# Performance work log

Measured on AMD Instinct MI355X. Metric: run time of the kernel, lower is better.

The kernel has to match this reference:

```python
import jax, jax.numpy as jnp
import numpy as np

N_NODES = 50000
N_RELS = 50
N_CLASSES = 40
EMB_DIM = 16
RP = 16
N_TRIPLES = 400000


def setup_inputs() -> dict:
    rng = np.random.default_rng(0)
    s = rng.integers(0, N_NODES, size=N_TRIPLES)
    r = rng.integers(0, N_RELS, size=N_TRIPLES)
    o = rng.integers(0, N_NODES, size=N_TRIPLES)
    # unique (s,o) pairs, as in torch.unique(pairs, dim=0, return_inverse=True)
    pairs = np.stack([s, o], axis=1)
    unique_pairs, inverse = np.unique(pairs, axis=0, return_inverse=True)
    nt = unique_pairs.shape[0]
    # relation_matrix COO (nt, num_rels), coalesced (duplicate (row,col) summed)
    keys = inverse.astype(np.int64) * N_RELS + r
    uk, counts = np.unique(keys, return_counts=True)
    rm_rows = (uk // N_RELS).astype(np.int32)
    rm_cols = (uk % N_RELS).astype(np.int32)
    rm_vals = counts.astype(np.float32)
    # hindices / vindices exactly as in __init__ (note o*rm / s*rm construction)
    s_u = unique_pairs[:, 0].astype(np.int64)
    o_u = unique_pairs[:, 1].astype(np.int64)
    rm = np.arange(RP, dtype=np.int64)[:, None]            # (rp, 1)
    h_rows = np.broadcast_to(s_u[None, :], (RP, nt)).reshape(-1).astype(np.int32)
    h_cols = (o_u[None, :] * rm).reshape(-1).astype(np.int32)
    v_rows = (s_u[None, :] * rm).reshape(-1).astype(np.int32)
    v_cols = np.broadcast_to(o_u[None, :], (RP, nt)).reshape(-1).astype(np.int32)
    # float params (xavier-like scale for weights, randn for rel emb, zero biases)
    key = jax.random.key(0)
    k1, k2, k3 = jax.random.split(key, 3)
    gain = np.sqrt(2.0)  # relu gain
    w1_std = gain * np.sqrt(2.0 / (N_NODES + EMB_DIM))
    w2_std = gain * np.sqrt(2.0 / (EMB_DIM + N_CLASSES))
    return {
        'rel_emb': jax.random.normal(k1, (N_RELS, RP), dtype=jnp.float32),
        'weights1': jax.random.normal(k2, (RP, N_NODES, EMB_DIM), dtype=jnp.float32) * w1_std,
        'weights2': jax.random.normal(k3, (RP, EMB_DIM, N_CLASSES), dtype=jnp.float32) * w2_std,
        'bias1': jnp.zeros((EMB_DIM,), dtype=jnp.float32),
        'bias2': jnp.zeros((N_CLASSES,), dtype=jnp.float32),
        'rm_rows': jnp.asarray(rm_rows),
        'rm_cols': jnp.asarray(rm_cols),
        'rm_vals': jnp.asarray(rm_vals),
        'h_rows': jnp.asarray(h_rows),
        'h_cols': jnp.asarray(h_cols),
        'v_rows': jnp.asarray(v_rows),
        'v_cols': jnp.asarray(v_cols),
    }


def reference(rel_emb, weights1, weights2, bias1, bias2,
              rm_rows, rm_cols, rm_vals, h_rows, h_cols, v_rows, v_cols):
    rp, n, e = weights1.shape
    nt = h_rows.shape[0] // rp
    # latents = sparse.mm(relation_matrix, relation_embeddings) -> (nt, rp)
    latents = jax.ops.segment_sum(rm_vals[:, None] * rel_emb[rm_cols], rm_rows,
                                  num_segments=nt)
    latents = jax.nn.softmax(latents, axis=1)
    lf = latents.T.reshape(-1)                              # (rp*nt,)
    # sum_sparse(hindices, lf, (n, n*rp), row=False): per-column sums, gathered
    colsum = jax.ops.segment_sum(lf, h_cols, num_segments=n * rp)
    ln = lf / colsum[h_cols]
    # spmm(hindices, ln, (n, n*rp), weights1_flat) -> (n, e)
    w1f = weights1.reshape(rp * n, e)
    h = jax.ops.segment_sum(ln[:, None] * w1f[h_cols], h_rows, num_segments=n)
    h = jax.nn.relu(h + bias1)
    # sum_sparse(vindices, lf, (n*rp, n), row=True): per-row sums, gathered
    rowsum = jax.ops.segment_sum(lf, v_rows, num_segments=n * rp)
    ln2 = lf / rowsum[v_rows]
    # spmm(vindices, ln2, (n*rp, n), h) -> (n*rp, e)
    h2 = jax.ops.segment_sum(ln2[:, None] * h[v_cols], v_rows, num_segments=n * rp)
    h2 = h2.reshape(rp, n, e)
    out = jnp.einsum('rhc,rnh->nc', weights2, h2) + bias2
    return out
```

## Files before the change

### kernel.cpp

```cpp
#include <hip/hip_runtime.h>

#define RP 16
#define EMB 16
#define NC 40

#define BCASTF(dst, srci, R) \
    dst = __int_as_float(__builtin_amdgcn_mov_dpp(srci, 0x150 + R, 0xf, 0xf, true));

__global__ void k_count(const int* __restrict__ s_u, const int* __restrict__ o_u,
                        int* __restrict__ cnt_s, int* __restrict__ cnt_o, int nt) {
    int t = blockIdx.x * blockDim.x + threadIdx.x;
    if (t < nt) {
        atomicAdd(&cnt_s[s_u[t]], 1);
        atomicAdd(&cnt_o[o_u[t]], 1);
    }
}

__global__ void k_scan_blk(const int* __restrict__ cnt_s, int* __restrict__ offs_s,
                           const int* __restrict__ cnt_o, int* __restrict__ offs_o,
                           int* __restrict__ partials, int n, int nblk) {
    const int* in = blockIdx.y ? cnt_o : cnt_s;
    int* out = blockIdx.y ? offs_o : offs_s;
    int tid = threadIdx.x;
    int i0 = blockIdx.x * 1024 + tid * 4;
    int v[4];
    #pragma unroll
    for (int q = 0; q < 4; ++q) {
        int i = i0 + q;
        v[q] = (i < n) ? in[i] : 0;
    }
    int tsum = v[0] + v[1] + v[2] + v[3];
    int lane = tid & 63, wid = tid >> 6;
    int x = tsum;
    #pragma unroll
    for (int d = 1; d < 64; d <<= 1) {
        int u = __shfl_up(x, d, 64);
        if (lane >= d) x += u;
    }
    __shared__ int wsum[4];
    if (lane == 63) wsum[wid] = x;
    __syncthreads();
    int woff = 0;
    for (int wq = 0; wq < wid; ++wq) woff += wsum[wq];
    int run = woff + x - tsum;
    #pragma unroll
    for (int q = 0; q < 4; ++q) {
        int i = i0 + q;
        if (i < n) out[i] = run;
        run += v[q];
    }
    if (tid == 255) partials[blockIdx.y * nblk + blockIdx.x] = run;
}

__global__ void k_scan_top(int* __restrict__ partials, int nblk) {
    int w = threadIdx.x >> 6;
    int lane = threadIdx.x & 63;
    int carry = 0;
    for (int base = 0; base < nblk; base += 64) {
        int idx = base + lane;
        int v = (idx < nblk) ? partials[w * nblk + idx] : 0;
        int x = v;
        #pragma unroll
        for (int d = 1; d < 64; d <<= 1) {
            int u = __shfl_up(x, d, 64);
            if (lane >= d) x += u;
        }
        if (idx < nblk) partials[w * nblk + idx] = carry + x - v;
        carry += __shfl(x, 63, 64);
    }
}

__global__ void k_scan_add(int* __restrict__ offs_s, int* __restrict__ cur_s,
                           int* __restrict__ offs_o, int* __restrict__ cur_o,
                           const int* __restrict__ partials, int n, int nblk) {
    int* out = blockIdx.y ? offs_o : offs_s;
    int* cur = blockIdx.y ? cur_o : cur_s;
    int add = partials[blockIdx.y * nblk + blockIdx.x];
    int i0 = blockIdx.x * 1024 + threadIdx.x * 4;
    #pragma unroll
    for (int q = 0; q < 4; ++q) {
        int i = i0 + q;
        if (i < n) {
            int vv = out[i] + add;
            out[i] = vv;
            cur[i] = vv;
        }
    }
}

__global__ void k_latents(const float* __restrict__ rel_emb,
                          const int* __restrict__ rows,
                          const int* __restrict__ cols,
                          const float* __restrict__ vals,
                          const int* __restrict__ s_u,
                          const int* __restrict__ o_u,
                          int* __restrict__ cur_o,
                          float* __restrict__ lat_t, float* __restrict__ lat_o,
                          float* __restrict__ lat0, int* __restrict__ su_o,
                          int nm) {
    int i = blockIdx.x * blockDim.x + threadIdx.x;
    int e = i >> 4, k = i & 15;
    if (e >= nm) return;
    int row = rows[e];
    if (e > 0 && rows[e - 1] == row) return;
    float acc = vals[e] * rel_emb[cols[e] * RP + k];
    while (e + 1 < nm && rows[e + 1] == row) {
        ++e;
        acc += vals[e] * rel_emb[cols[e] * RP + k];
    }
    float m = acc;
    #pragma unroll
    for (int d = 1; d < 16; d <<= 1) m = fmaxf(m, __shfl_xor(m, d, 16));
    float v = expf(acc - m);
    float s = v;
    #pragma unroll
    for (int d = 1; d < 16; d <<= 1) s += __shfl_xor(s, d, 16);
    v = v / s;
    lat_t[(size_t)row * RP + k] = v;
    int po = 0;
    if (k == 0) {
        int ou = o_u[row];
        po = atomicAdd(&cur_o[ou], 1);
        su_o[po] = s_u[row];
        lat0[row] = v;
    }
    po = __shfl(po, 0, 16);
    lat_o[(size_t)po * RP + k] = v;
}

__global__ void k_r0(const float* __restrict__ lat0,
                     float* __restrict__ rowsum, float* __restrict__ colsum,
                     int nt) {
    float acc = 0.f;
    for (int t = blockIdx.x * blockDim.x + threadIdx.x; t < nt;
         t += gridDim.x * blockDim.x)
        acc += lat0[t];
    #pragma unroll
    for (int d = 32; d; d >>= 1) acc += __shfl_down(acc, d, 64);
    __shared__ float sm[4];
    int lane = threadIdx.x & 63, wid = threadIdx.x >> 6;
    if (lane == 0) sm[wid] = acc;
    __syncthreads();
    if (threadIdx.x == 0) {
        float tot = sm[0] + sm[1] + sm[2] + sm[3];
        atomicAdd(&rowsum[0], tot);
        atomicAdd(&colsum[0], tot);
    }
}

__global__ void k_latsum(const float* __restrict__ lat_o,
                         const int* __restrict__ offs_o,
                         const int* __restrict__ cnt_o,
                         float* __restrict__ colsum, int n) {
    int i = blockIdx.x * blockDim.x + threadIdx.x;
    int v = i >> 4, k = i & 15;
    if (v >= n) return;
    int beg = offs_o[v], d = cnt_o[v];
    if (d == 0) return;
    float ls = 0.f;
    int j = 0;
    for (; j + 4 <= d; j += 4) {
        float a0 = lat_o[(size_t)(beg + j + 0) * RP + k];
        float a1 = lat_o[(size_t)(beg + j + 1) * RP + k];
        float a2 = lat_o[(size_t)(beg + j + 2) * RP + k];
        float a3 = lat_o[(size_t)(beg + j + 3) * RP + k];
        ls += (a0 + a1) + (a2 + a3);
    }
    for (; j < d; ++j) ls += lat_o[(size_t)(beg + j) * RP + k];
    if (k >= 1) atomicAdd(&colsum[(size_t)v * k], ls);
}

__global__ void k_h_acc(const float* __restrict__ lat_o,
                        const int* __restrict__ offs_o,
                        const int* __restrict__ cnt_o,
                        const int* __restrict__ su_o,
                        const float* __restrict__ colsum,
                        const float* __restrict__ w1,
                        float* __restrict__ h, int n) {
    int i = blockIdx.x * blockDim.x + threadIdx.x;
    int o = i >> 4, k = i & 15;
    if (o >= n) return;
    int d = cnt_o[o];
    if (d == 0) return;
    int beg = offs_o[o];
    float W[RP];
    #pragma unroll
    for (int r = 0; r < RP; ++r)
        W[r] = w1[(size_t)(o * r) * EMB + k];
    float rcp_cs = 1.f / colsum[(size_t)o * k];
    for (int j0 = 0; j0 < d; j0 += 16) {
        int su16 = su_o[beg + min(j0 + k, d - 1)];
        float la[16];
        #pragma unroll
        for (int e = 0; e < 16; ++e)
            la[e] = lat_o[(size_t)(beg + min(j0 + e, d - 1)) * RP + k];
        #pragma unroll
        for (int e = 0; e < 16; ++e) {
            if (j0 + e >= d) break;
            float ln = la[e] * rcp_cs;
            int ln_i = __float_as_int(ln);
            float acc = 0.f, b;
            #define HACC_STEP(R) BCASTF(b, ln_i, R); acc = fmaf(b, W[R], acc);
            HACC_STEP(0)  HACC_STEP(1)  HACC_STEP(2)  HACC_STEP(3)
            HACC_STEP(4)  HACC_STEP(5)  HACC_STEP(6)  HACC_STEP(7)
            HACC_STEP(8)  HACC_STEP(9)  HACC_STEP(10) HACC_STEP(11)
            HACC_STEP(12) HACC_STEP(13) HACC_STEP(14) HACC_STEP(15)
            #undef HACC_STEP
            int s = __shfl(su16, e, 16);
            atomicAdd(&h[s * EMB + k], acc);
        }
    }
}

__global__ void k_h2(const float* __restrict__ lat_t,
                     const int* __restrict__ offs_s,
                     const int* __restrict__ cnt_s,
                     const int* __restrict__ o_u,
                     float* __restrict__ rowsum,
                     const float* __restrict__ h,
                     const float* __restrict__ bias1,
                     float* __restrict__ M2,
                     float* __restrict__ r0part, int n) {
    __shared__ float r0acc[EMB];
    if (threadIdx.x < EMB) r0acc[threadIdx.x] = 0.f;
    __syncthreads();
    int i = blockIdx.x * blockDim.x + threadIdx.x;
    int s = i >> 4, k = i & 15;
    float b1k = bias1[k];
    float M[RP];
    #pragma unroll
    for (int r = 0; r < RP; ++r) M[r] = 0.f;
    float rs_acc = 0.f;
    int d = 0;
    if (s < n) {
        int beg = offs_s[s];
        d = cnt_s[s];
        for (int j0 = 0; j0 < d; j0 += 16) {
            int o16 = o_u[beg + min(j0 + k, d - 1)];
            float hv[16], la[16];
            #pragma unroll
            for (int e = 0; e < 16; ++e) {
                int oe = __shfl(o16, e, 16);
                hv[e] = h[(size_t)oe * EMB + k];
                la[e] = lat_t[(size_t)(beg + min(j0 + e, d - 1)) * RP + k];
            }
            #pragma unroll
            for (int e = 0; e < 16; ++e) {
                if (j0 + e >= d) break;
                float hvr = fmaxf(hv[e] + b1k, 0.f);
                rs_acc += la[e];
                int lat_i = __float_as_int(la[e]);
                float b;
                #define H2_STEP(R) BCASTF(b, lat_i, R); M[R] = fmaf(b, hvr, M[R]);
                H2_STEP(0)  H2_STEP(1)  H2_STEP(2)  H2_STEP(3)
                H2_STEP(4)  H2_STEP(5)  H2_STEP(6)  H2_STEP(7)
                H2_STEP(8)  H2_STEP(9)  H2_STEP(10) H2_STEP(11)
                H2_STEP(12) H2_STEP(13) H2_STEP(14) H2_STEP(15)
                #undef H2_STEP
            }
        }
    }
    if (s < n) {
        if (d > 0) {
            if (k >= 1) atomicAdd(&rowsum[(size_t)s * k], rs_acc);
            atomicAdd(&r0acc[k], M[0]);
        }
        float* dst = &M2[(size_t)s * 15 * EMB + k];
        #pragma unroll
        for (int r = 1; r < RP; ++r)
            dst[(size_t)(r - 1) * EMB] = M[r];
    }
    __syncthreads();
    if (threadIdx.x < EMB)
        r0part[(size_t)blockIdx.x * EMB + threadIdx.x] = r0acc[threadIdx.x];
}

__global__ void k_h2r0(const float* __restrict__ r0part,
                       float* __restrict__ g0, int nblk) {
    __shared__ float red[1024];
    int k = threadIdx.x & 15, j0 = threadIdx.x >> 4;
    float acc = 0.f;
    for (int j = j0; j < nblk; j += 64)
        acc += r0part[(size_t)j * EMB + k];
    red[j0 * 16 + k] = acc;
    __syncthreads();
    #pragma unroll
    for (int st = 32; st >= 1; st >>= 1) {
        if (j0 < st) red[j0 * 16 + k] += red[(j0 + st) * 16 + k];
        __syncthreads();
    }
    if (threadIdx.x < 16) g0[threadIdx.x] = red[threadIdx.x];
}

#define CB2 20
__global__ void k_out(const float* __restrict__ w2,
                      const float* __restrict__ bias2,
                      const float* __restrict__ M2,
                      const float* __restrict__ g0,
                      const float* __restrict__ rowsum,
                      float* __restrict__ out, int n) {
    __shared__ float w2s[RP * EMB * NC];
    for (int i = threadIdx.x; i < RP * EMB * NC; i += 256)
        w2s[i] = w2[i];
    __syncthreads();
    int gi = blockIdx.x * blockDim.x + threadIdx.x;
    int node = gi >> 1;
    int c0 = (gi & 1) * CB2;
    if (node >= n) return;
    float acc[CB2];
    #pragma unroll
    for (int c = 0; c < CB2; ++c) acc[c] = bias2[c0 + c];
    for (int rq = 0; rq < RP; ++rq) {
        int m = rq * n + node;
        float rs = rowsum[m];
        float rcp = (rs != 0.f) ? 1.f / rs : 0.f;
        float hv[EMB];
        #pragma unroll
        for (int q = 0; q < EMB; ++q) hv[q] = 0.f;
        if (m == 0) {
            #pragma unroll
            for (int q = 0; q < EMB; ++q) hv[q] = g0[q];
        }
        #pragma unroll
        for (int r = 1; r < RP; ++r) {
            if (m % r == 0) {
                int s = m / r;
                if (s < n) {
                    const float4* row =
                        (const float4*)&M2[((size_t)s * 15 + (r - 1)) * EMB];
                    #pragma unroll
                    for (int q = 0; q < 4; ++q) {
                        float4 v = row[q];
                        hv[q * 4 + 0] += v.x;
                        hv[q * 4 + 1] += v.y;
                        hv[q * 4 + 2] += v.z;
                        hv[q * 4 + 3] += v.w;
                    }
                }
            }
        }
        #pragma unroll
        for (int hh = 0; hh < EMB; ++hh) {
            const float4* wrow = (const float4*)&w2s[(rq * EMB + hh) * NC + c0];
            float hvv = hv[hh] * rcp;
            #pragma unroll
            for (int q5 = 0; q5 < 5; ++q5) {
                float4 wv = wrow[q5];
                acc[q5 * 4 + 0] += wv.x * hvv;
                acc[q5 * 4 + 1] += wv.y * hvv;
                acc[q5 * 4 + 2] += wv.z * hvv;
                acc[q5 * 4 + 3] += wv.w * hvv;
            }
        }
    }
    float4* op = (float4*)&out[node * NC + c0];
    #pragma unroll
    for (int q5 = 0; q5 < 5; ++q5)
        op[q5] = make_float4(acc[q5 * 4], acc[q5 * 4 + 1],
                             acc[q5 * 4 + 2], acc[q5 * 4 + 3]);
}

extern "C" void kernel_launch(void* const* d_in, const int* in_sizes, int n_in,
                              void* d_out, int out_size, void* d_ws, size_t ws_size,
                              hipStream_t stream) {
    const float* rel_emb = (const float*)d_in[0];
    const float* w1      = (const float*)d_in[1];
    const float* w2      = (const float*)d_in[2];
    const float* b1      = (const float*)d_in[3];
    const float* b2      = (const float*)d_in[4];
    const int*   rm_rows = (const int*)d_in[5];
    const int*   rm_cols = (const int*)d_in[6];
    const float* rm_vals = (const float*)d_in[7];
    const int*   h_rows  = (const int*)d_in[8];
    const int*   v_cols  = (const int*)d_in[11];

    const int nm = in_sizes[5];
    const int ne = in_sizes[8];
    const int nt = ne / RP;
    const int n  = in_sizes[1] / (RP * EMB);

    const int B = 256;
    const int nblk_h2 = (n * 16 + B - 1) / B;
    const int nblk_sc = (n + 1023) / 1024;

    char* w = (char*)d_ws;
    float* colsum = (float*)w;  w += (size_t)n * RP * 4;
    float* rowsum = (float*)w;  w += (size_t)n * RP * 4;
    float* h      = (float*)w;  w += (size_t)n * EMB * 4;
    int* cnt_s    = (int*)w;    w += (size_t)n * 4;
    int* cnt_o    = (int*)w;    w += (size_t)n * 4;
    size_t zero_bytes = (size_t)(w - (char*)d_ws);
    float* M2     = (float*)w;  w += (size_t)n * 15 * EMB * 4;
    float* lat_t  = (float*)w;  w += (size_t)nt * RP * 4;
    float* lat_o  = (float*)w;  w += (size_t)nt * RP * 4;
    float* lat0   = (float*)w;  w += (size_t)nt * 4;
    int* su_o     = (int*)w;    w += (size_t)nt * 4;
    int* offs_s   = (int*)w;    w += (size_t)n * 4;
    int* cur_s    = (int*)w;    w += (size_t)n * 4;
    int* offs_o   = (int*)w;    w += (size_t)n * 4;
    int* cur_o    = (int*)w;    w += (size_t)n * 4;
    float* r0part = (float*)w;  w += (size_t)nblk_h2 * EMB * 4;
    float* g0     = (float*)w;  w += (size_t)EMB * 4;
    int* partials = (int*)w;    w += (size_t)2 * nblk_sc * 4;
    if ((size_t)(w - (char*)d_ws) > ws_size) return;

    hipMemsetAsync(d_ws, 0, zero_bytes, stream);

    k_count<<<dim3((nt + B - 1) / B), dim3(B), 0, stream>>>(
        h_rows, v_cols, cnt_s, cnt_o, nt);
    k_scan_blk<<<dim3(nblk_sc, 2), dim3(B), 0, stream>>>(
        cnt_s, offs_s, cnt_o, offs_o, partials, n, nblk_sc);
    k_scan_top<<<dim3(1), dim3(128), 0, stream>>>(partials, nblk_sc);
    k_scan_add<<<dim3(nblk_sc, 2), dim3(B), 0, stream>>>(
        offs_s, cur_s, offs_o, cur_o, partials, n, nblk_sc);
    k_latents<<<dim3((nm * 16 + B - 1) / B), dim3(B), 0, stream>>>(
        rel_emb, rm_rows, rm_cols, rm_vals, h_rows, v_cols,
        cur_o, lat_t, lat_o, lat0, su_o, nm);
    k_r0<<<dim3(64), dim3(B), 0, stream>>>(lat0, rowsum, colsum, nt);
    k_latsum<<<dim3((n * 16 + B - 1) / B), dim3(B), 0, stream>>>(
        lat_o, offs_o, cnt_o, colsum, n);
    k_h_acc<<<dim3((n * 16 + B - 1) / B), dim3(B), 0, stream>>>(
        lat_o, offs_o, cnt_o, su_o, colsum, w1, h, n);
    k_h2<<<dim3(nblk_h2), dim3(B), 0, stream>>>(
        lat_t, offs_s, cnt_s, v_cols, rowsum, h, b1, M2, r0part, n);
    k_h2r0<<<dim3(1), dim3(1024), 0, stream>>>(r0part, g0, nblk_h2);
    k_out<<<dim3((n * 2 + B - 1) / B), dim3(B), 0, stream>>>(
        w2, b2, M2, g0, rowsum, (float*)d_out, n);
}
```

Measured before the change: 271.9 us.

## Remap k_out to 16 lanes per node with DPP broadcast of hidden values

The output kernel now gives each node 16 threads, one per embedding component, instead of 2 threads that each cover 20 classes. Each lane loads one M2 element, scales it by the reciprocal row sum, and uses DPP row broadcasts to share the 16 hidden values. Each lane then accumulates up to 3 output classes. This cuts per-thread registers and serial FMA work and makes M2 loads coalesced, at the cost of 8x more threads, redundant rowsum and mod/div work per lane, and some idle lanes on the third class.

```diff
diff --git a/kernel.cpp b/kernel.cpp
--- a/kernel.cpp
+++ b/kernel.cpp
@@ -292,7 +292,6 @@
     if (threadIdx.x < 16) g0[threadIdx.x] = red[threadIdx.x];
 }
 
-#define CB2 20
 __global__ void k_out(const float* __restrict__ w2,
                       const float* __restrict__ bias2,
                       const float* __restrict__ M2,
@@ -304,60 +303,42 @@
         w2s[i] = w2[i];
     __syncthreads();
     int gi = blockIdx.x * blockDim.x + threadIdx.x;
-    int node = gi >> 1;
-    int c0 = (gi & 1) * CB2;
+    int node = gi >> 4, k = gi & 15;
     if (node >= n) return;
-    float acc[CB2];
-    #pragma unroll
-    for (int c = 0; c < CB2; ++c) acc[c] = bias2[c0 + c];
+    int c2 = (k < 8) ? (k + 32) : 39;
+    float acc0 = bias2[k];
+    float acc1 = bias2[k + 16];
+    float acc2 = (k < 8) ? bias2[k + 32] : 0.f;
     for (int rq = 0; rq < RP; ++rq) {
         int m = rq * n + node;
-        float rs = rowsum[m];
-        float rcp = (rs != 0.f) ? 1.f / rs : 0.f;
-        float hv[EMB];
-        #pragma unroll
-        for (int q = 0; q < EMB; ++q) hv[q] = 0.f;
-        if (m == 0) {
-            #pragma unroll
-            for (int q = 0; q < EMB; ++q) hv[q] = g0[q];
-        }
+        float hv = (m == 0) ? g0[k] : 0.f;
         #pragma unroll
         for (int r = 1; r < RP; ++r) {
             if (m % r == 0) {
                 int s = m / r;
-                if (s < n) {
-                    const float4* row =
-                        (const float4*)&M2[((size_t)s * 15 + (r - 1)) * EMB];
-                    #pragma unroll
-                    for (int q = 0; q < 4; ++q) {
-                        float4 v = row[q];
-                        hv[q * 4 + 0] += v.x;
-                        hv[q * 4 + 1] += v.y;
-                        hv[q * 4 + 2] += v.z;
-                        hv[q * 4 + 3] += v.w;
-                    }
-                }
+                if (s < n)
+                    hv += M2[((size_t)s * 15 + (r - 1)) * EMB + k];
             }
         }
-        #pragma unroll
-        for (int hh = 0; hh < EMB; ++hh) {
-            const float4* wrow = (const float4*)&w2s[(rq * EMB + hh) * NC + c0];
-            float hvv = hv[hh] * rcp;
-            #pragma unroll
-            for (int q5 = 0; q5 < 5; ++q5) {
-                float4 wv = wrow[q5];
-                acc[q5 * 4 + 0] += wv.x * hvv;
-                acc[q5 * 4 + 1] += wv.y * hvv;
-                acc[q5 * 4 + 2] += wv.z * hvv;
-                acc[q5 * 4 + 3] += wv.w * hvv;
-            }
-        }
-    }
-    float4* op = (float4*)&out[node * NC + c0];
-    #pragma unroll
-    for (int q5 = 0; q5 < 5; ++q5)
-        op[q5] = make_float4(acc[q5 * 4], acc[q5 * 4 + 1],
-                             acc[q5 * 4 + 2], acc[q5 * 4 + 3]);
+        float rs = rowsum[m];
+        float rcp = (rs != 0.f) ? 1.f / rs : 0.f;
+        hv *= rcp;
+        int hv_i = __float_as_int(hv);
+        const float* wbase = &w2s[rq * EMB * NC];
+        float b;
+        #define OUT_STEP(H) BCASTF(b, hv_i, H); \
+            acc0 = fmaf(b, wbase[H * NC + k], acc0); \
+            acc1 = fmaf(b, wbase[H * NC + k + 16], acc1); \
+            acc2 = fmaf(b, wbase[H * NC + c2], acc2);
+        OUT_STEP(0)  OUT_STEP(1)  OUT_STEP(2)  OUT_STEP(3)
+        OUT_STEP(4)  OUT_STEP(5)  OUT_STEP(6)  OUT_STEP(7)
+        OUT_STEP(8)  OUT_STEP(9)  OUT_STEP(10) OUT_STEP(11)
+        OUT_STEP(12) OUT_STEP(13) OUT_STEP(14) OUT_STEP(15)
+        #undef OUT_STEP
+    }
+    out[node * NC + k] = acc0;
+    out[node * NC + k + 16] = acc1;
+    if (k < 8) out[node * NC + k + 32] = acc2;
 }
 
 extern "C" void kernel_launch(void* const* d_in, const int* in_sizes, int n_in,
@@ -424,6 +405,6 @@
     k_h2<<<dim3(nblk_h2), dim3(B), 0, stream>>>(
         lat_t, offs_s, cnt_s, v_cols, rowsum, h, b1, M2, r0part, n);
     k_h2r0<<<dim3(1), dim3(1024), 0, stream>>>(r0part, g0, nblk_h2);
-    k_out<<<dim3((n * 2 + B - 1) / B), dim3(B), 0, stream>>>(
+    k_out<<<dim3((n * 16 + B - 1) / B), dim3(B), 0, stream>>>(
         w2, b2, M2, g0, rowsum, (float*)d_out, n);
 }
```

Measured after the change: 345.1 us. 26.9% more time.

## Restructure output kernel to scatter M2 rows into shared strips per node tile

Applied to the files above, without the earlier changes.

Instead of each thread testing divisibility of m by every r and gathering M2 rows, each block now owns a strip of 128 nodes and, for each rq, computes the range of source rows s whose products s*r fall in the strip. It scatters those rows into a shared-memory strip with LDS atomics, then applies the w2 contraction from shared memory. This removes the per-thread integer divisions and the divergent, scattered gathers, and makes the M2 reads more coalesced. In exchange it adds block-wide syncs and LDS atomics on every rq iteration, plus more shared memory per block.

```diff
diff --git a/kernel.cpp b/kernel.cpp
--- a/kernel.cpp
+++ b/kernel.cpp
@@ -3,6 +3,7 @@
 #define RP 16
 #define EMB 16
 #define NC 40
+#define LSTRIP 128
 
 #define BCASTF(dst, srci, R) \
     dst = __int_as_float(__builtin_amdgcn_mov_dpp(srci, 0x150 + R, 0xf, 0xf, true));
@@ -292,7 +293,6 @@
     if (threadIdx.x < 16) g0[threadIdx.x] = red[threadIdx.x];
 }
 
-#define CB2 20
 __global__ void k_out(const float* __restrict__ w2,
                       const float* __restrict__ bias2,
                       const float* __restrict__ M2,
@@ -300,64 +300,68 @@
                       const float* __restrict__ rowsum,
                       float* __restrict__ out, int n) {
     __shared__ float w2s[RP * EMB * NC];
-    for (int i = threadIdx.x; i < RP * EMB * NC; i += 256)
+    __shared__ float strip[LSTRIP * EMB];
+    __shared__ float rsq[LSTRIP];
+    int tid = threadIdx.x;
+    for (int i = tid; i < RP * EMB * NC; i += 256)
         w2s[i] = w2[i];
-    __syncthreads();
-    int gi = blockIdx.x * blockDim.x + threadIdx.x;
-    int node = gi >> 1;
-    int c0 = (gi & 1) * CB2;
-    if (node >= n) return;
-    float acc[CB2];
-    #pragma unroll
-    for (int c = 0; c < CB2; ++c) acc[c] = bias2[c0 + c];
+    int v0 = blockIdx.x * LSTRIP;
+    int L = min(LSTRIP, n - v0);
+    int node_l = tid >> 1;
+    int c0 = (tid & 1) * 20;
+    float acc[20];
+    #pragma unroll
+    for (int c = 0; c < 20; ++c) acc[c] = bias2[c0 + c];
+    int g = tid >> 4, k = tid & 15;
     for (int rq = 0; rq < RP; ++rq) {
-        int m = rq * n + node;
-        float rs = rowsum[m];
-        float rcp = (rs != 0.f) ? 1.f / rs : 0.f;
-        float hv[EMB];
-        #pragma unroll
-        for (int q = 0; q < EMB; ++q) hv[q] = 0.f;
-        if (m == 0) {
+        __syncthreads();
+        for (int i = tid; i < LSTRIP * EMB; i += 256) strip[i] = 0.f;
+        if (tid < LSTRIP) {
+            float rs = (tid < L) ? rowsum[(size_t)rq * n + v0 + tid] : 0.f;
+            rsq[tid] = (rs != 0.f) ? 1.f / rs : 0.f;
+        }
+        __syncthreads();
+        int m0 = rq * n + v0;
+        int mhi = m0 + L - 1;
+        #pragma unroll
+        for (int r = 1; r < RP; ++r) {
+            int slo = (m0 + r - 1) / r;
+            int shi = min(n - 1, mhi / r);
+            for (int s = slo + g; s <= shi; s += 16) {
+                float v = M2[((size_t)s * 15 + (r - 1)) * EMB + k];
+                atomicAdd(&strip[(s * r - m0) * EMB + k], v);
+            }
+        }
+        __syncthreads();
+        if (rq == 0 && v0 == 0 && tid < EMB)
+            strip[tid] += g0[tid];
+        __syncthreads();
+        if (node_l < L) {
+            float rcp = rsq[node_l];
+            const float* srow = &strip[node_l * EMB];
+            const float* wbase = &w2s[rq * EMB * NC];
             #pragma unroll
-            for (int q = 0; q < EMB; ++q) hv[q] = g0[q];
-        }
-        #pragma unroll
-        for (int r = 1; r < RP; ++r) {
-            if (m % r == 0) {
-                int s = m / r;
-                if (s < n) {
-                    const float4* row =
-                        (const float4*)&M2[((size_t)s * 15 + (r - 1)) * EMB];
-                    #pragma unroll
-                    for (int q = 0; q < 4; ++q) {
-                        float4 v = row[q];
-                        hv[q * 4 + 0] += v.x;
-                        hv[q * 4 + 1] += v.y;
-                        hv[q * 4 + 2] += v.z;
-                        hv[q * 4 + 3] += v.w;
-                    }
+            for (int hh = 0; hh < EMB; ++hh) {
+                float hv = srow[hh] * rcp;
+                const float4* wrow = (const float4*)&wbase[hh * NC + c0];
+                #pragma unroll
+                for (int q5 = 0; q5 < 5; ++q5) {
+                    float4 wv = wrow[q5];
+                    acc[q5 * 4 + 0] = fmaf(wv.x, hv, acc[q5 * 4 + 0]);
+                    acc[q5 * 4 + 1] = fmaf(wv.y, hv, acc[q5 * 4 + 1]);
+                    acc[q5 * 4 + 2] = fmaf(wv.z, hv, acc[q5 * 4 + 2]);
+                    acc[q5 * 4 + 3] = fmaf(wv.w, hv, acc[q5 * 4 + 3]);
                 }
             }
         }
-        #pragma unroll
-        for (int hh = 0; hh < EMB; ++hh) {
-            const float4* wrow = (const float4*)&w2s[(rq * EMB + hh) * NC + c0];
-            float hvv = hv[hh] * rcp;
-            #pragma unroll
-            for (int q5 = 0; q5 < 5; ++q5) {
-                float4 wv = wrow[q5];
-                acc[q5 * 4 + 0] += wv.x * hvv;
-                acc[q5 * 4 + 1] += wv.y * hvv;
-                acc[q5 * 4 + 2] += wv.z * hvv;
-                acc[q5 * 4 + 3] += wv.w * hvv;
-            }
-        }
-    }
-    float4* op = (float4*)&out[node * NC + c0];
-    #pragma unroll
-    for (int q5 = 0; q5 < 5; ++q5)
-        op[q5] = make_float4(acc[q5 * 4], acc[q5 * 4 + 1],
-                             acc[q5 * 4 + 2], acc[q5 * 4 + 3]);
+    }
+    if (node_l < L) {
+        float4* op = (float4*)&out[(size_t)(v0 + node_l) * NC + c0];
+        #pragma unroll
+        for (int q5 = 0; q5 < 5; ++q5)
+            op[q5] = make_float4(acc[q5 * 4], acc[q5 * 4 + 1],
+                                 acc[q5 * 4 + 2], acc[q5 * 4 + 3]);
+    }
 }
 
 extern "C" void kernel_launch(void* const* d_in, const int* in_sizes, int n_in,
@@ -424,6 +428,6 @@
     k_h2<<<dim3(nblk_h2), dim3(B), 0, stream>>>(
         lat_t, offs_s, cnt_s, v_cols, rowsum, h, b1, M2, r0part, n);
     k_h2r0<<<dim3(1), dim3(1024), 0, stream>>>(r0part, g0, nblk_h2);
-    k_out<<<dim3((n * 2 + B - 1) / B), dim3(B), 0, stream>>>(
+    k_out<<<dim3((n + LSTRIP - 1) / LSTRIP), dim3(B), 0, stream>>>(
         w2, b2, M2, g0, rowsum, (float*)d_out, n);
 }
```

After: 324.0 us. +19.2%, slower.
